# Kernel optimization log

Hardware: AMD Instinct MI355X
Metric: run time of the kernel (lower is better)

Reference implementation:

```python
import jax, jax.numpy as jnp
import numpy as np

D = 256; N_GRU = 4; L = 3; RATIO = 0.8; B = 64; PAD = 0
VOCAB = 50000; N = 20000; E = 320000; T = 16


def setup_inputs() -> dict:
    key = jax.random.key(0)
    ks = jax.random.split(key, 10)
    s = 0.05
    return {
        "x_tokens": jax.random.randint(ks[0], (N, T), 0, VOCAB),
        "edge_index": jax.random.randint(ks[1], (2, E), 0, N),
        "batch": jnp.sort(jax.random.randint(ks[2], (N,), 0, B)),
        "embed": jax.random.normal(ks[3], (VOCAB, D)) * s,
        "ggc_W": jax.random.normal(ks[4], (L, N_GRU, D, D)) * s,
        "gru_Wih": jax.random.normal(ks[5], (L, 3 * D, D)) * s,
        "gru_Whh": jax.random.normal(ks[6], (L, 3 * D, D)) * s,
        "gru_bih": jnp.zeros((L, 3 * D)),
        "gru_bhh": jnp.zeros((L, 3 * D)),
        "topk_p": jax.random.normal(ks[7], (L, D)) * s,
        "gate_W": jax.random.normal(ks[8], (D, 1)) * s,
        "gate_b": jnp.zeros((1,)),
    }


def gru_cell(m, h, Wih, Whh, bih, bhh):
    gi = m @ Wih.T + bih
    gh = h @ Whh.T + bhh
    i_r, i_z, i_n = jnp.split(gi, 3, axis=-1)
    h_r, h_z, h_n = jnp.split(gh, 3, axis=-1)
    r = jax.nn.sigmoid(i_r + h_r)
    z = jax.nn.sigmoid(i_z + h_z)
    n = jnp.tanh(i_n + r * h_n)
    return (1.0 - z) * n + z * h


def gated_graph_conv(h, src, dst, emask, W, Wih, Whh, bih, bhh):
    # PyG GatedGraphConv: per step, transform then scatter-add source->target, then GRU update
    for l in range(N_GRU):
        msg = (h @ W[l])[src] * emask[:, None]            # [E, D]
        agg = jax.ops.segment_sum(msg, dst, num_segments=h.shape[0])
        h = gru_cell(agg, h, Wih, Whh, bih, bhh)
    return h


def topk_pool(x, p, nmask, batch, src, dst, emask):
    # PyG TopKPooling: score = tanh(x.p/||p||), keep top ceil(ratio*n) per graph, x *= score
    score = jnp.tanh((x @ p) / jnp.linalg.norm(p))
    skey = jnp.where(nmask, score, -1e9)
    order = jnp.lexsort((-skey, batch))                   # by graph asc, score desc
    counts = jax.ops.segment_sum(jnp.ones((N,), jnp.int32), batch, num_segments=B)
    starts = jnp.cumsum(counts) - counts
    rank = jnp.zeros((N,), jnp.int32).at[order].set(
        jnp.arange(N, dtype=jnp.int32) - starts[batch[order]])
    n_valid = jax.ops.segment_sum(nmask.astype(jnp.int32), batch, num_segments=B)
    k = jnp.ceil(RATIO * n_valid.astype(jnp.float32)).astype(jnp.int32)
    keep = nmask & (rank < k[batch])
    x_new = jnp.where(keep[:, None], x * score[:, None], 0.0)
    emask_new = emask * keep[src].astype(emask.dtype) * keep[dst].astype(emask.dtype)
    return x_new, keep, emask_new


def global_att(x, nmask, batch, gW, gb):
    # GlobalAttention: segment softmax of Linear(x,1), weighted sum per graph
    logit = jnp.where(nmask, (x @ gW)[:, 0] + gb[0], -1e9)
    mx = jax.ops.segment_max(logit, batch, num_segments=B)
    e = jnp.where(nmask, jnp.exp(logit - mx[batch]), 0.0)
    denom = jax.ops.segment_sum(e, batch, num_segments=B)
    gate = e / jnp.maximum(denom[batch], 1e-12)
    return jax.ops.segment_sum(gate[:, None] * x, batch, num_segments=B)


def reference(x_tokens, edge_index, batch, embed, ggc_W, gru_Wih, gru_Whh,
              gru_bih, gru_bhh, topk_p, gate_W, gate_b):
    # STEncoder: embed token ids, mean-pool non-pad tokens per node
    tok_mask = (x_tokens != PAD)
    emb = embed[x_tokens] * tok_mask[..., None]
    h = emb.sum(1) / jnp.maximum(tok_mask.sum(1, keepdims=True), 1).astype(emb.dtype)
    src, dst = edge_index[0], edge_index[1]
    nmask = jnp.ones((N,), bool)
    emask = jnp.ones((E,), h.dtype)
    out = jnp.zeros((B, D), h.dtype)
    for l in range(L):
        h = jax.nn.relu(gated_graph_conv(h, src, dst, emask, ggc_W[l],
                                         gru_Wih[l], gru_Whh[l], gru_bih[l], gru_bhh[l]))
        h, nmask, emask = topk_pool(h, topk_p[l], nmask, batch, src, dst, emask)
        out = out + global_att(h, nmask, batch, gate_W, gate_b)
    return out
```

## Files before the change

kernel.cpp:

```cpp
#include <hip/hip_runtime.h>
#include <hip/hip_bf16.h>

namespace {

constexpr int NN = 20000;
constexpr int TT = 16;
constexpr int DD = 256;
constexpr int EE = 320000;
constexpr int BB = 64;
constexpr int NLAY = 3;
constexpr int NGRUS = 4;
constexpr int D3 = 768;
constexpr int NRB = 157;
constexpr int NXCD = 8;

typedef __bf16 bf16x8 __attribute__((ext_vector_type(8)));
typedef float  f32x4  __attribute__((ext_vector_type(4)));

__device__ __forceinline__ float us2f(unsigned short u){
  union { unsigned int i; float f; } v; v.i = ((unsigned int)u) << 16; return v.f;
}
__device__ __forceinline__ unsigned short f2us(float f){
  union { float f; unsigned int i; } v; v.f = f;
  unsigned int r = v.i + 0x7fff + ((v.i >> 16) & 1);
  return (unsigned short)(r >> 16);
}

__device__ __forceinline__ void gload16(const unsigned short* g, unsigned short* l){
  __builtin_amdgcn_global_load_lds(
      (const __attribute__((address_space(1))) unsigned int*)g,
      (__attribute__((address_space(3))) unsigned int*)l, 16, 0, 0);
}

__global__ void k_init(int* __restrict__ deg, int* __restrict__ cursor,
                       int* __restrict__ nmask, float* __restrict__ out){
  int i = blockIdx.x*256 + threadIdx.x;
  if (i < NN){ deg[i] = 0; cursor[i] = 0; nmask[i] = 1; }
  if (i < BB*DD) out[i] = 0.f;
}

__global__ void k_embed(const int* __restrict__ xt, const float* __restrict__ emb,
                        unsigned short* __restrict__ h){
  int n = blockIdx.x; int d = threadIdx.x;
  __shared__ int toks[TT];
  if (threadIdx.x < TT) toks[threadIdx.x] = xt[n*TT + threadIdx.x];
  __syncthreads();
  float acc = 0.f; int cnt = 0;
  #pragma unroll
  for (int t = 0; t < TT; ++t){
    int tk = toks[t];
    if (tk != 0){ ++cnt; acc += emb[(size_t)tk*DD + d]; }
  }
  h[(size_t)n*DD + d] = f2us(acc / (float)(cnt > 0 ? cnt : 1));
}

__global__ __launch_bounds__(256) void k_wf(const float* __restrict__ W,
                                            const float* __restrict__ Wih,
                                            unsigned short* __restrict__ WFThi,
                                            unsigned short* __restrict__ WFTlo){
  int lg = blockIdx.z; int l = lg / NGRUS;
  const float* A  = W   + (size_t)lg*DD*DD;
  const float* Bm = Wih + (size_t)l*D3*DD;
  unsigned short* oh = WFThi + (size_t)lg*D3*DD;
  unsigned short* ol = WFTlo + (size_t)lg*D3*DD;
  int k0 = blockIdx.y*64, j0 = blockIdx.x*64;
  __shared__ float sA[16][68], sB[16][68];
  int tid = threadIdx.x, ty = tid/16, tx = tid%16;
  float acc[4][4] = {};
  int m = tid >> 2, dg = (tid & 3)*4;
  for (int d0 = 0; d0 < DD; d0 += 16){
    float4 ua = *reinterpret_cast<const float4*>(A  + (size_t)(k0+m)*DD + d0+dg);
    float4 ub = *reinterpret_cast<const float4*>(Bm + (size_t)(j0+m)*DD + d0+dg);
    __syncthreads();
    sA[dg+0][m]=ua.x; sA[dg+1][m]=ua.y; sA[dg+2][m]=ua.z; sA[dg+3][m]=ua.w;
    sB[dg+0][m]=ub.x; sB[dg+1][m]=ub.y; sB[dg+2][m]=ub.z; sB[dg+3][m]=ub.w;
    __syncthreads();
    #pragma unroll
    for (int dd = 0; dd < 16; ++dd){
      float a[4], b[4];
      #pragma unroll
      for (int i=0;i<4;++i) a[i] = sA[dd][ty*4+i];
      #pragma unroll
      for (int j=0;j<4;++j) b[j] = sB[dd][tx*4+j];
      #pragma unroll
      for (int i=0;i<4;++i)
        #pragma unroll
        for (int j=0;j<4;++j) acc[i][j] += a[i]*b[j];
    }
  }
  for (int i=0;i<4;++i){
    int k = k0 + ty*4 + i;
    for (int j=0;j<4;++j){
      int c = j0 + tx*4 + j;
      float v = acc[i][j];
      unsigned short hi = f2us(v);
      float rem = v - us2f(hi);
      oh[(size_t)c*DD + k] = hi;
      ol[(size_t)c*DD + k] = f2us(rem);
    }
  }
}

__global__ void k_whh_split(const float* __restrict__ Whh, unsigned short* __restrict__ hi,
                            unsigned short* __restrict__ lo){
  size_t i = (size_t)blockIdx.x*256 + threadIdx.x;
  if (i >= (size_t)NLAY*D3*DD) return;
  float w = Whh[i];
  unsigned short h = f2us(w);
  hi[i] = h; lo[i] = f2us(w - us2f(h));
}

__global__ void k_deg(const int* __restrict__ dst, int* __restrict__ deg){
  int e = blockIdx.x*256 + threadIdx.x; if (e < EE) atomicAdd(&deg[dst[e]], 1);
}
__global__ void k_scan(const int* __restrict__ deg, int* __restrict__ offs){
  __shared__ int part[1024];
  int t = threadIdx.x; const int CH = 20;
  int base = t*CH; int s = 0;
  for (int i = 0; i < CH; ++i){ int idx = base+i; if (idx < NN) s += deg[idx]; }
  part[t] = s; __syncthreads();
  for (int o = 1; o < 1024; o <<= 1){
    int v = part[t]; int add = (t >= o) ? part[t-o] : 0;
    __syncthreads(); part[t] = v + add; __syncthreads();
  }
  int run = (t > 0) ? part[t-1] : 0;
  for (int i = 0; i < CH; ++i){ int idx = base+i; if (idx < NN){ offs[idx] = run; run += deg[idx]; } }
  if (t == 1023) offs[NN] = run;
}
__global__ void k_fill_csr(const int* __restrict__ src, const int* __restrict__ dst,
                           const int* __restrict__ offs, int* __restrict__ cursor,
                           int* __restrict__ csr_src){
  int e = blockIdx.x*256 + threadIdx.x; if (e >= EE) return;
  int d = dst[e]; int pos = atomicAdd(&cursor[d], 1);
  csr_src[offs[d] + pos] = src[e];
}

__global__ void k_bounds(const int* __restrict__ batch, int* __restrict__ starts65){
  int n = blockIdx.x*256 + threadIdx.x;
  if (n >= NN) return;
  int b = batch[n];
  int p = (n == 0) ? -1 : batch[n-1];
  for (int bb = p+1; bb <= b; ++bb) starts65[bb] = n;
  if (n == NN-1){
    for (int bb = b+1; bb <= BB; ++bb) starts65[bb] = NN;
  }
}
__global__ void k_cnts(const int* __restrict__ starts65, int* __restrict__ counts){
  int b = threadIdx.x;
  if (b < BB) counts[b] = starts65[b+1] - starts65[b];
}

__global__ void k_agg(const unsigned short* __restrict__ h, const int* __restrict__ offs,
                      const int* __restrict__ csr_src, unsigned short* __restrict__ agg){
  int wid = threadIdx.x >> 6, lane = threadIdx.x & 63;
  int n = blockIdx.x*4 + wid;
  if (n >= NN) return;
  int s = offs[n], e = offs[n+1];
  float a0 = 0.f, a1 = 0.f, a2 = 0.f, a3 = 0.f;
  int slot = s;
  for (; slot + 2 <= e; slot += 2){
    int s0 = csr_src[slot], s1 = csr_src[slot+1];
    ushort4 v0 = *reinterpret_cast<const ushort4*>(h + (size_t)s0*DD + lane*4);
    ushort4 v1 = *reinterpret_cast<const ushort4*>(h + (size_t)s1*DD + lane*4);
    a0 += us2f(v0.x) + us2f(v1.x);
    a1 += us2f(v0.y) + us2f(v1.y);
    a2 += us2f(v0.z) + us2f(v1.z);
    a3 += us2f(v0.w) + us2f(v1.w);
  }
  if (slot < e){
    int s0 = csr_src[slot];
    ushort4 v0 = *reinterpret_cast<const ushort4*>(h + (size_t)s0*DD + lane*4);
    a0 += us2f(v0.x); a1 += us2f(v0.y); a2 += us2f(v0.z); a3 += us2f(v0.w);
  }
  ushort4 o;
  o.x = f2us(a0); o.y = f2us(a1); o.z = f2us(a2); o.w = f2us(a3);
  *reinterpret_cast<ushort4*>(agg + (size_t)n*DD + lane*4) = o;
}

__global__ __launch_bounds__(256) void k_gru(
    const unsigned short* __restrict__ Ag, const unsigned short* __restrict__ Ah,
    const unsigned short* __restrict__ WfH, const unsigned short* __restrict__ WfL,
    const unsigned short* __restrict__ WhH, const unsigned short* __restrict__ WhL,
    const float* __restrict__ bih, const float* __restrict__ bhh,
    const int* __restrict__ nmask, unsigned short* __restrict__ Hn, int do_relu){
  __shared__ unsigned short sB[2][96*64];
  int t = threadIdx.x;
  int wv = t >> 6, lane = t & 63;
  int lr = lane & 15, kg = lane >> 4;

  int w = blockIdx.x;
  int q = (w & 7)*NRB + (w >> 3);
  int r0 = (q >> 3) * 128;
  int g0 = q & 7;

  int sw   = ((lane & 7) ^ (lane >> 3)) * 8;
  int rloc = lane >> 3;

  auto stageB = [&](int buf, int p){
    int a = p >> 1;
    const unsigned short* m = (p & 1) ? ((a & 4) ? WhL : WfL)
                                      : ((a & 4) ? WhH : WfH);
    int kin0 = (a & 3) * 64;
    #pragma unroll
    for (int i = 0; i < 3; ++i){
      int brow = (wv + i*4)*8;
      int gate = brow >> 5;
      int srcrow = gate*256 + g0*32 + (brow & 31) + rloc;
      gload16(m + (size_t)srcrow*DD + kin0 + sw, &sB[buf][brow*64]);
    }
  };

  f32x4 aR[2][2], aZ[2][2], aNi[2][2], aNh[2][2];
  #pragma unroll
  for (int rf = 0; rf < 2; ++rf)
    #pragma unroll
    for (int h2 = 0; h2 < 2; ++h2){
      aR[rf][h2] = (f32x4){0.f,0.f,0.f,0.f};  aZ[rf][h2] = (f32x4){0.f,0.f,0.f,0.f};
      aNi[rf][h2] = (f32x4){0.f,0.f,0.f,0.f}; aNh[rf][h2] = (f32x4){0.f,0.f,0.f,0.f};
    }

  size_t arow0 = (size_t)(r0 + wv*32 + lr) * DD;
  size_t arow1 = (size_t)(r0 + wv*32 + 16 + lr) * DD;

  stageB(0, 0);
  #pragma unroll
  for (int a = 0; a < 8; ++a){
    const unsigned short* Asrc = (a & 4) ? Ah : Ag;
    int kin0 = (a & 3) * 64;
    bf16x8 aF0[2], aF1[2];
    #pragma unroll
    for (int kk2 = 0; kk2 < 2; ++kk2){
      aF0[kk2] = *reinterpret_cast<const bf16x8*>(Asrc + arow0 + kin0 + kk2*32 + kg*8);
      aF1[kk2] = *reinterpret_cast<const bf16x8*>(Asrc + arow1 + kin0 + kk2*32 + kg*8);
    }
    int half = (a >> 2) & 1;
    #pragma unroll
    for (int ph = 0; ph < 2; ++ph){
      int p = a*2 + ph;
      int bbuf = p & 1;
      __syncthreads();
      if (p < 15) stageB(bbuf ^ 1, p + 1);
      #pragma unroll
      for (int kk2 = 0; kk2 < 2; ++kk2){
        int cs = ((kk2*4 + kg) ^ (lr & 7)) * 8;
        bf16x8 a0 = aF0[kk2];
        bf16x8 a1 = aF1[kk2];
        #pragma unroll
        for (int h2 = 0; h2 < 2; ++h2){
          bf16x8 bR = *reinterpret_cast<const bf16x8*>(&sB[bbuf][(      h2*16 + lr)*64 + cs]);
          bf16x8 bZ = *reinterpret_cast<const bf16x8*>(&sB[bbuf][(32  + h2*16 + lr)*64 + cs]);
          bf16x8 bN = *reinterpret_cast<const bf16x8*>(&sB[bbuf][(64  + h2*16 + lr)*64 + cs]);
          aR[0][h2] = __builtin_amdgcn_mfma_f32_16x16x32_bf16(a0, bR, aR[0][h2], 0, 0, 0);
          aR[1][h2] = __builtin_amdgcn_mfma_f32_16x16x32_bf16(a1, bR, aR[1][h2], 0, 0, 0);
          aZ[0][h2] = __builtin_amdgcn_mfma_f32_16x16x32_bf16(a0, bZ, aZ[0][h2], 0, 0, 0);
          aZ[1][h2] = __builtin_amdgcn_mfma_f32_16x16x32_bf16(a1, bZ, aZ[1][h2], 0, 0, 0);
          if (half){
            aNh[0][h2] = __builtin_amdgcn_mfma_f32_16x16x32_bf16(a0, bN, aNh[0][h2], 0, 0, 0);
            aNh[1][h2] = __builtin_amdgcn_mfma_f32_16x16x32_bf16(a1, bN, aNh[1][h2], 0, 0, 0);
          } else {
            aNi[0][h2] = __builtin_amdgcn_mfma_f32_16x16x32_bf16(a0, bN, aNi[0][h2], 0, 0, 0);
            aNi[1][h2] = __builtin_amdgcn_mfma_f32_16x16x32_bf16(a1, bN, aNi[1][h2], 0, 0, 0);
          }
        }
      }
    }
  }

  #pragma unroll
  for (int h2 = 0; h2 < 2; ++h2){
    int col = g0*32 + h2*16 + lr;
    float bRv = bih[col]       + bhh[col];
    float bZv = bih[256 + col] + bhh[256 + col];
    float bN1 = bih[512 + col];
    float bN2 = bhh[512 + col];
    #pragma unroll
    for (int rf = 0; rf < 2; ++rf){
      #pragma unroll
      for (int j = 0; j < 4; ++j){
        int row = r0 + wv*32 + rf*16 + kg*4 + j;
        if (row < NN){
          float r = 1.f/(1.f + expf(-(aR[rf][h2][j] + bRv)));
          float z = 1.f/(1.f + expf(-(aZ[rf][h2][j] + bZv)));
          float nv = tanhf(aNi[rf][h2][j] + bN1 + r*(aNh[rf][h2][j] + bN2));
          float ho = us2f(Ah[(size_t)row*DD + col]);
          float o = (1.f - z)*nv + z*ho;
          if (do_relu) o = fmaxf(o, 0.f);
          if (!nmask[row]) o = 0.f;
          Hn[(size_t)row*DD + col] = f2us(o);
        }
      }
    }
  }
}

__global__ void k_score(const unsigned short* __restrict__ h, const float* __restrict__ p,
                        float* __restrict__ score){
  int wid = threadIdx.x >> 6, lane = threadIdx.x & 63;
  int n = blockIdx.x*4 + wid; if (n >= NN) return;
  ushort4 hu = *reinterpret_cast<const ushort4*>(h + (size_t)n*DD + lane*4);
  float4 pv = *reinterpret_cast<const float4*>(p + lane*4);
  float dot = us2f(hu.x)*pv.x + us2f(hu.y)*pv.y + us2f(hu.z)*pv.z + us2f(hu.w)*pv.w;
  float pp = pv.x*pv.x + pv.y*pv.y + pv.z*pv.z + pv.w*pv.w;
  for (int o = 32; o; o >>= 1){ dot += __shfl_down(dot, o); pp += __shfl_down(pp, o); }
  if (lane == 0) score[n] = tanhf(dot / sqrtf(pp));
}

__global__ void k_topk(const float* __restrict__ score, const int* __restrict__ starts,
                       const int* __restrict__ counts, int* __restrict__ nmask){
  int b = blockIdx.x; int st = starts[b]; int cnt = min(counts[b], 1024);
  __shared__ float sc[1024]; __shared__ int ired[256];
  int t = threadIdx.x;
  int myvalid = 0;
  for (int i = t; i < cnt; i += 256){
    int node = st + i; int v = nmask[node];
    sc[i] = v ? score[node] : -1e30f;
    myvalid += v;
  }
  ired[t] = myvalid; __syncthreads();
  for (int o = 128; o; o >>= 1){ if (t < o) ired[t] += ired[t+o]; __syncthreads(); }
  int nv = ired[0];
  int k = (4*nv + 4)/5;
  __syncthreads();
  for (int i = t; i < cnt; i += 256){
    float si = sc[i]; int node = st + i; int keep = 0;
    if (si > -1e29f){
      int rank = 0;
      for (int j = 0; j < cnt; ++j){
        float sj = sc[j];
        rank += (sj > si) || (sj == si && j < i);
      }
      keep = (rank < k);
    }
    nmask[node] = keep;
  }
}

__global__ void k_scale(unsigned short* __restrict__ h, const float* __restrict__ score,
                        const int* __restrict__ nmask){
  int idx = blockIdx.x*256 + threadIdx.x;
  int n = idx >> 8;
  unsigned short v = nmask[n] ? f2us(us2f(h[idx])*score[n]) : (unsigned short)0;
  h[idx] = v;
}

__global__ void k_att(const unsigned short* __restrict__ h, const float* __restrict__ gW,
                      const float* __restrict__ gb, const int* __restrict__ starts,
                      const int* __restrict__ counts, const int* __restrict__ nmask,
                      float* __restrict__ outacc){
  int b = blockIdx.x; int st = starts[b]; int cnt = min(counts[b], 1024);
  __shared__ float lg[1024]; __shared__ float red[256];
  int t = threadIdx.x, wid = t >> 6, lane = t & 63;
  float gbv = gb[0];
  for (int i = wid; i < cnt; i += 4){
    int node = st + i;
    ushort4 hu = *reinterpret_cast<const ushort4*>(h + (size_t)node*DD + lane*4);
    float4 wv = *reinterpret_cast<const float4*>(gW + lane*4);
    float dot = us2f(hu.x)*wv.x + us2f(hu.y)*wv.y + us2f(hu.z)*wv.z + us2f(hu.w)*wv.w;
    for (int o = 32; o; o >>= 1) dot += __shfl_down(dot, o);
    if (lane == 0) lg[i] = nmask[node] ? dot + gbv : -1e30f;
  }
  __syncthreads();
  float mx = -1e30f;
  for (int i = t; i < cnt; i += 256) mx = fmaxf(mx, lg[i]);
  red[t] = mx; __syncthreads();
  for (int o = 128; o; o >>= 1){ if (t < o) red[t] = fmaxf(red[t], red[t+o]); __syncthreads(); }
  mx = red[0]; __syncthreads();
  float se = 0.f;
  for (int i = t; i < cnt; i += 256){
    float e = (lg[i] > -1e29f) ? expf(lg[i] - mx) : 0.f;
    lg[i] = e; se += e;
  }
  red[t] = se; __syncthreads();
  for (int o = 128; o; o >>= 1){ if (t < o) red[t] += red[t+o]; __syncthreads(); }
  float denom = fmaxf(red[0], 1e-12f);
  __syncthreads();
  float a0=0.f,a1=0.f,a2=0.f,a3=0.f;
  int i = 0;
  for (; i + 4 <= cnt; i += 4){
    a0 += lg[i+0]*us2f(h[(size_t)(st+i+0)*DD + t]);
    a1 += lg[i+1]*us2f(h[(size_t)(st+i+1)*DD + t]);
    a2 += lg[i+2]*us2f(h[(size_t)(st+i+2)*DD + t]);
    a3 += lg[i+3]*us2f(h[(size_t)(st+i+3)*DD + t]);
  }
  for (; i < cnt; ++i) a0 += lg[i]*us2f(h[(size_t)(st+i)*DD + t]);
  outacc[(size_t)b*DD + t] += (a0+a1+a2+a3)/denom;
}

}

extern "C" void kernel_launch(void* const* d_in, const int* in_sizes, int n_in,
                              void* d_out, int out_size, void* d_ws, size_t ws_size,
                              hipStream_t stream){
  const int*   x_tokens = (const int*)d_in[0];
  const int*   e_src    = (const int*)d_in[1];
  const int*   e_dst    = e_src + EE;
  const int*   batch    = (const int*)d_in[2];
  const float* embed    = (const float*)d_in[3];
  const float* ggcW     = (const float*)d_in[4];
  const float* gWih     = (const float*)d_in[5];
  const float* gWhh     = (const float*)d_in[6];
  const float* gbih     = (const float*)d_in[7];
  const float* gbhh     = (const float*)d_in[8];
  const float* topkp    = (const float*)d_in[9];
  const float* gateW    = (const float*)d_in[10];
  const float* gateb    = (const float*)d_in[11];
  (void)in_sizes; (void)n_in; (void)out_size;
  float* out = (float*)d_out;

  char* ws = (char*)d_ws;
  size_t off = 0;
  auto carve = [&](size_t bytes)->char*{
    char* p = ws + off;
    off += (bytes + 255) & ~(size_t)255;
    return p;
  };
  unsigned short* h0    = (unsigned short*)carve((size_t)NN*DD*2);
  unsigned short* h1    = (unsigned short*)carve((size_t)NN*DD*2);
  unsigned short* agg   = (unsigned short*)carve((size_t)NN*DD*2);
  unsigned short* WFThi = (unsigned short*)carve((size_t)NLAY*NGRUS*D3*DD*2);
  unsigned short* WFTlo = (unsigned short*)carve((size_t)NLAY*NGRUS*D3*DD*2);
  unsigned short* WhhHi = (unsigned short*)carve((size_t)NLAY*D3*DD*2);
  unsigned short* WhhLo = (unsigned short*)carve((size_t)NLAY*D3*DD*2);
  float* score   = (float*)carve((size_t)NN*4);
  int* nmask     = (int*)carve((size_t)NN*4);
  int* deg       = (int*)carve((size_t)NN*4);
  int* cursor    = (int*)carve((size_t)NN*4);
  int* offs      = (int*)carve((size_t)(NN+1)*4);
  int* csr_src   = (int*)carve((size_t)EE*4);
  int* counts    = (int*)carve((size_t)BB*4);
  int* starts    = (int*)carve((size_t)(BB+1)*4);
  if (off > ws_size) return;

  k_init<<<(NN+255)/256, 256, 0, stream>>>(deg, cursor, nmask, out);
  k_embed<<<NN, DD, 0, stream>>>(x_tokens, embed, h0);
  k_wf<<<dim3(D3/64, DD/64, NLAY*NGRUS), 256, 0, stream>>>(ggcW, gWih, WFThi, WFTlo);
  k_whh_split<<<(NLAY*D3*DD + 255)/256, 256, 0, stream>>>(gWhh, WhhHi, WhhLo);
  k_deg<<<(EE+255)/256, 256, 0, stream>>>(e_dst, deg);
  k_scan<<<1, 1024, 0, stream>>>(deg, offs);
  k_fill_csr<<<(EE+255)/256, 256, 0, stream>>>(e_src, e_dst, offs, cursor, csr_src);
  k_bounds<<<(NN+255)/256, 256, 0, stream>>>(batch, starts);
  k_cnts<<<1, 64, 0, stream>>>(starts, counts);

  unsigned short* hc = h0; unsigned short* hn = h1;
  for (int l = 0; l < NLAY; ++l){
    const unsigned short* WhHl = WhhHi + (size_t)l*D3*DD;
    const unsigned short* WhLl = WhhLo + (size_t)l*D3*DD;
    const float* bihl = gbih + (size_t)l*D3;
    const float* bhhl = gbhh + (size_t)l*D3;
    for (int g = 0; g < NGRUS; ++g){
      const unsigned short* WfHl = WFThi + (size_t)(l*NGRUS+g)*D3*DD;
      const unsigned short* WfLl = WFTlo + (size_t)(l*NGRUS+g)*D3*DD;
      k_agg<<<(NN+3)/4, 256, 0, stream>>>(hc, offs, csr_src, agg);
      k_gru<<<NRB*NXCD, 256, 0, stream>>>(agg, hc, WfHl, WfLl, WhHl, WhLl,
                                          bihl, bhhl, nmask, hn,
                                          (g == NGRUS-1) ? 1 : 0);
      unsigned short* tmp = hc; hc = hn; hn = tmp;
    }
    k_score<<<NN/4, 256, 0, stream>>>(hc, topkp + (size_t)l*DD, score);
    k_topk<<<BB, 256, 0, stream>>>(score, starts, counts, nmask);
    k_scale<<<NN, 256, 0, stream>>>(hc, score, nmask);
    k_att<<<BB, 256, 0, stream>>>(hc, gateW, gateb, starts, counts, nmask, out);
  }
}
```

Before: 1.343 ms.

## Stage both weight halves per step and prefetch next A fragments in GRU GEMM

The GRU GEMM kernel now stages both the high and low weight tiles for one K-chunk into a doubled shared buffer at once. This halves the number of __syncthreads barriers per K step. It also prefetches the next chunk's A fragments into registers (double-buffered) while the current chunk computes, and raises wave priority around the MFMA block. Shared memory use doubles and register pressure rises, which may reduce occupancy.

New measurement: 1.374 ms. 2.3% more time.

```diff
diff --git a/kernel.cpp b/kernel.cpp
--- a/kernel.cpp
+++ b/kernel.cpp
@@ -183,7 +183,7 @@
     const unsigned short* __restrict__ WhH, const unsigned short* __restrict__ WhL,
     const float* __restrict__ bih, const float* __restrict__ bhh,
     const int* __restrict__ nmask, unsigned short* __restrict__ Hn, int do_relu){
-  __shared__ unsigned short sB[2][96*64];
+  __shared__ unsigned short sB[2][2][96*64];
   int t = threadIdx.x;
   int wv = t >> 6, lane = t & 63;
   int lr = lane & 15, kg = lane >> 4;
@@ -196,17 +196,17 @@
   int sw   = ((lane & 7) ^ (lane >> 3)) * 8;
   int rloc = lane >> 3;
 
-  auto stageB = [&](int buf, int p){
-    int a = p >> 1;
-    const unsigned short* m = (p & 1) ? ((a & 4) ? WhL : WfL)
-                                      : ((a & 4) ? WhH : WfH);
+  auto stageBoth = [&](int buf, int a){
+    const unsigned short* mH = (a & 4) ? WhH : WfH;
+    const unsigned short* mL = (a & 4) ? WhL : WfL;
     int kin0 = (a & 3) * 64;
     #pragma unroll
     for (int i = 0; i < 3; ++i){
       int brow = (wv + i*4)*8;
       int gate = brow >> 5;
-      int srcrow = gate*256 + g0*32 + (brow & 31) + rloc;
-      gload16(m + (size_t)srcrow*DD + kin0 + sw, &sB[buf][brow*64]);
+      size_t srow = (size_t)(gate*256 + g0*32 + (brow & 31) + rloc)*DD + kin0 + sw;
+      gload16(mH + srow, &sB[buf][0][brow*64]);
+      gload16(mL + srow, &sB[buf][1][brow*64]);
     }
   };
 
@@ -222,34 +222,43 @@
   size_t arow0 = (size_t)(r0 + wv*32 + lr) * DD;
   size_t arow1 = (size_t)(r0 + wv*32 + 16 + lr) * DD;
 
-  stageB(0, 0);
+  bf16x8 aF0[2][2], aF1[2][2];
+  #pragma unroll
+  for (int kk2 = 0; kk2 < 2; ++kk2){
+    aF0[0][kk2] = *reinterpret_cast<const bf16x8*>(Ag + arow0 + kk2*32 + kg*8);
+    aF1[0][kk2] = *reinterpret_cast<const bf16x8*>(Ag + arow1 + kk2*32 + kg*8);
+  }
+  stageBoth(0, 0);
+
   #pragma unroll
   for (int a = 0; a < 8; ++a){
-    const unsigned short* Asrc = (a & 4) ? Ah : Ag;
-    int kin0 = (a & 3) * 64;
-    bf16x8 aF0[2], aF1[2];
-    #pragma unroll
-    for (int kk2 = 0; kk2 < 2; ++kk2){
-      aF0[kk2] = *reinterpret_cast<const bf16x8*>(Asrc + arow0 + kin0 + kk2*32 + kg*8);
-      aF1[kk2] = *reinterpret_cast<const bf16x8*>(Asrc + arow1 + kin0 + kk2*32 + kg*8);
+    int buf = a & 1;
+    int par = a & 1;
+    __syncthreads();
+    if (a < 7){
+      stageBoth(buf ^ 1, a + 1);
+      const unsigned short* An = ((a+1) & 4) ? Ah : Ag;
+      int kinn = ((a+1) & 3) * 64;
+      #pragma unroll
+      for (int kk2 = 0; kk2 < 2; ++kk2){
+        aF0[par ^ 1][kk2] = *reinterpret_cast<const bf16x8*>(An + arow0 + kinn + kk2*32 + kg*8);
+        aF1[par ^ 1][kk2] = *reinterpret_cast<const bf16x8*>(An + arow1 + kinn + kk2*32 + kg*8);
+      }
     }
     int half = (a >> 2) & 1;
+    __builtin_amdgcn_s_setprio(1);
     #pragma unroll
     for (int ph = 0; ph < 2; ++ph){
-      int p = a*2 + ph;
-      int bbuf = p & 1;
-      __syncthreads();
-      if (p < 15) stageB(bbuf ^ 1, p + 1);
       #pragma unroll
       for (int kk2 = 0; kk2 < 2; ++kk2){
         int cs = ((kk2*4 + kg) ^ (lr & 7)) * 8;
-        bf16x8 a0 = aF0[kk2];
-        bf16x8 a1 = aF1[kk2];
+        bf16x8 a0 = aF0[par][kk2];
+        bf16x8 a1 = aF1[par][kk2];
         #pragma unroll
         for (int h2 = 0; h2 < 2; ++h2){
-          bf16x8 bR = *reinterpret_cast<const bf16x8*>(&sB[bbuf][(      h2*16 + lr)*64 + cs]);
-          bf16x8 bZ = *reinterpret_cast<const bf16x8*>(&sB[bbuf][(32  + h2*16 + lr)*64 + cs]);
-          bf16x8 bN = *reinterpret_cast<const bf16x8*>(&sB[bbuf][(64  + h2*16 + lr)*64 + cs]);
+          bf16x8 bR = *reinterpret_cast<const bf16x8*>(&sB[buf][ph][(      h2*16 + lr)*64 + cs]);
+          bf16x8 bZ = *reinterpret_cast<const bf16x8*>(&sB[buf][ph][(32  + h2*16 + lr)*64 + cs]);
+          bf16x8 bN = *reinterpret_cast<const bf16x8*>(&sB[buf][ph][(64  + h2*16 + lr)*64 + cs]);
           aR[0][h2] = __builtin_amdgcn_mfma_f32_16x16x32_bf16(a0, bR, aR[0][h2], 0, 0, 0);
           aR[1][h2] = __builtin_amdgcn_mfma_f32_16x16x32_bf16(a1, bR, aR[1][h2], 0, 0, 0);
           aZ[0][h2] = __builtin_amdgcn_mfma_f32_16x16x32_bf16(a0, bZ, aZ[0][h2], 0, 0, 0);
@@ -264,6 +273,7 @@
         }
       }
     }
+    __builtin_amdgcn_s_setprio(0);
   }
 
   #pragma unroll
```
